# Performance work log

Hardware: AMD Instinct MI355X
Metric: run time of the kernel (lower is better)

The kernel has to match this reference:

```python
import jax, jax.numpy as jnp
import numpy as np

D_MODEL = 1024
NUM_HEADS = 16
DEPTH = D_MODEL // NUM_HEADS


def setup_inputs() -> dict:
    key = jax.random.key(0)
    ks = jax.random.split(key, 8)
    B, S, D = 2, 2048, D_MODEL
    s = 1.0 / np.sqrt(D)
    return {
        "q": jax.random.normal(ks[0], (B, S, D), jnp.float32),
        "k": jax.random.normal(ks[1], (B, S, D), jnp.float32),
        "v": jax.random.normal(ks[2], (B, S, D), jnp.float32),
        "Wq": jax.random.normal(ks[3], (D, D), jnp.float32) * s,
        "bq": jnp.zeros((D,), jnp.float32),
        "Wk": jax.random.normal(ks[4], (D, D), jnp.float32) * s,
        "bk": jnp.zeros((D,), jnp.float32),
        "Wv": jax.random.normal(ks[5], (D, D), jnp.float32) * s,
        "bv": jnp.zeros((D,), jnp.float32),
        "Wo": jax.random.normal(ks[6], (D, D), jnp.float32) * s,
        "bo": jnp.zeros((D,), jnp.float32),
    }


def _split_heads(x):
    # [B,S,D] -> [B,H,S,depth]
    B, S, _ = x.shape
    return x.reshape(B, S, NUM_HEADS, DEPTH).transpose(0, 2, 1, 3)


def reference(q, k, v, Wq, bq, Wk, bk, Wv, bv, Wo, bo):
    qh = _split_heads(q @ Wq + bq)  # [B,H,S,d]
    kh = _split_heads(k @ Wk + bk)
    vh = _split_heads(v @ Wv + bv)
    scale = 1.0 / jnp.sqrt(jnp.float32(DEPTH))
    logits = jnp.einsum("bhqd,bhkd->bhqk", qh, kh) * scale  # [B,H,S,S]
    weights = jax.nn.softmax(logits, axis=-1)
    attn = jnp.einsum("bhqk,bhkd->bhqd", weights, vh)
    B, H, S, d = attn.shape
    attn = attn.transpose(0, 2, 1, 3).reshape(B, S, H * d)  # [B,S,D]
    return attn @ Wo + bo
```

## Files before the change

### kernel.cpp

```cpp
#include <hip/hip_runtime.h>
#include <hip/hip_bf16.h>
#include <stdint.h>


typedef __attribute__((ext_vector_type(8))) short bf16x8;
typedef __attribute__((ext_vector_type(4))) float f32x4;

#define MFMA16(a, b, c) __builtin_amdgcn_mfma_f32_16x16x32_bf16((a), (b), (c), 0, 0, 0)
#define EXP2(x) __builtin_amdgcn_exp2f(x)

static constexpr int S_LEN = 2048;
static constexpr int DM    = 1024;
static constexpr int DEPTH = 64;
static constexpr float QSCALE = 0.125f * 1.44269504088896340736f;

__device__ __forceinline__ unsigned short f2b(float f) {
  unsigned u = __float_as_uint(f);
  unsigned r = 0x7FFFu + ((u >> 16) & 1u);
  return (unsigned short)((u + r) >> 16);
}

__device__ __forceinline__ unsigned short b16(float f) {
  __hip_bfloat16 h = __float2bfloat16(f);
  union { __hip_bfloat16 h; unsigned short u; } c; c.h = h; return c.u;
}

__device__ __forceinline__ void gload16(const void* g, void* l) {
  __builtin_amdgcn_global_load_lds(
      (const __attribute__((address_space(1))) void*)g,
      (__attribute__((address_space(3))) void*)l, 16, 0, 0);
}

__device__ __forceinline__ void wave_lds_fence() {
  asm volatile("" ::: "memory");
  __builtin_amdgcn_sched_barrier(0);
}

__global__ __launch_bounds__(256) void prep_k(
    const float* __restrict__ xq, const float* __restrict__ xk,
    const float* __restrict__ xv, unsigned short* __restrict__ Xb,
    const float* __restrict__ Wq, const float* __restrict__ Wk,
    const float* __restrict__ Wv, const float* __restrict__ Wo,
    unsigned short* __restrict__ Wt) {
  __shared__ unsigned short ts[64][68];
  const int bid = blockIdx.x;
  const int tid = threadIdx.x;
  if (bid < 6144) {
    const int which = bid >> 11;
    const int xb = bid & 2047;
    const float* X = (which == 0) ? xq : (which == 1) ? xk : xv;
    size_t gid = ((size_t)xb * 256 + tid) * 8;
    float4 v0 = *(const float4*)&X[gid];
    float4 v1 = *(const float4*)&X[gid + 4];
    union { unsigned short u[8]; bf16x8 v; } pk;
    pk.u[0] = f2b(v0.x); pk.u[1] = f2b(v0.y); pk.u[2] = f2b(v0.z); pk.u[3] = f2b(v0.w);
    pk.u[4] = f2b(v1.x); pk.u[5] = f2b(v1.y); pk.u[6] = f2b(v1.z); pk.u[7] = f2b(v1.w);
    *(bf16x8*)&Xb[(size_t)which * 4096 * DM + gid] = pk.v;
    return;
  }
  const int wb = bid - 6144;
  const int w = wb >> 8, tile = wb & 255;
  const int tr = tile >> 4, tc = tile & 15;
  const float* W = (w == 0) ? Wq : (w == 1) ? Wk : (w == 2) ? Wv : Wo;
  unsigned short* T = Wt + (size_t)w * DM * DM;
  const int kr = tid >> 4, nc = (tid & 15) * 4;
  #pragma unroll
  for (int j = 0; j < 4; ++j) {
    int k = tr * 64 + kr + j * 16;
    float4 v = *(const float4*)&W[(size_t)k * DM + tc * 64 + nc];
    ushort4 u; u.x = f2b(v.x); u.y = f2b(v.y); u.z = f2b(v.z); u.w = f2b(v.w);
    *(ushort4*)&ts[kr + j * 16][nc] = u;
  }
  __syncthreads();
  const int nr = tid >> 4, kc = (tid & 15) * 4;
  #pragma unroll
  for (int j = 0; j < 4; ++j) {
    int n = tc * 64 + nr + j * 16;
    ushort4 u;
    u.x = ts[kc + 0][nr + j * 16];
    u.y = ts[kc + 1][nr + j * 16];
    u.z = ts[kc + 2][nr + j * 16];
    u.w = ts[kc + 3][nr + j * 16];
    *(ushort4*)&T[(size_t)n * DM + tr * 64 + kc] = u;
  }
}

__global__ __launch_bounds__(256, 4) void proj_qkv_k(
    const unsigned short* __restrict__ Xb, const unsigned short* __restrict__ Wt,
    const float* __restrict__ bq, const float* __restrict__ bk, const float* __restrict__ bv,
    unsigned short* __restrict__ Qh, unsigned short* __restrict__ Kh,
    unsigned short* __restrict__ Vt) {
  __shared__ __align__(16) unsigned short As[2][128][32];
  __shared__ __align__(16) unsigned short Bs[2][128][32];

  const int z = blockIdx.z;
  const unsigned short* A  = Xb + (size_t)z * 4096 * DM;
  const unsigned short* Bt = Wt + (size_t)z * DM * DM;
  const float* bias = (z == 0) ? bq : (z == 1) ? bk : bv;
  const float scale = (z == 0) ? QSCALE : 1.0f;
  unsigned short* O = (z == 0) ? Qh : (z == 1) ? Kh : Vt;

  const int bm = blockIdx.x, bn = blockIdx.y;
  const int tid = threadIdx.x;
  const int wave = tid >> 6, lane = tid & 63;
  const int wr = wave >> 1, wc = wave & 1;
  const int g = lane >> 4, i16 = lane & 15;
  const int srow = tid >> 2, sslot = tid & 3;

  f32x4 acc[4][4] = {};

  auto stage = [&](int ks, int buf) {
    #pragma unroll
    for (int rnd = 0; rnd < 2; ++rnd) {
      int row = rnd * 64 + srow;
      int sw = sslot ^ ((row >> 1) & 3);
      gload16(&A[(size_t)(bm * 128 + row) * DM + ks * 32 + sw * 8],
              &As[buf][row][sslot * 8]);
      gload16(&Bt[(size_t)(bn * 128 + row) * DM + ks * 32 + sw * 8],
              &Bs[buf][row][sslot * 8]);
    }
  };
  auto compute = [&](int buf) {
    bf16x8 a[4], b[4];
    #pragma unroll
    for (int m = 0; m < 4; ++m) {
      int row = wr * 64 + m * 16 + i16;
      int sl = g ^ ((row >> 1) & 3);
      a[m] = *(const bf16x8*)&As[buf][row][sl * 8];
    }
    #pragma unroll
    for (int n = 0; n < 4; ++n) {
      int row = wc * 64 + n * 16 + i16;
      int sl = g ^ ((row >> 1) & 3);
      b[n] = *(const bf16x8*)&Bs[buf][row][sl * 8];
    }
    #pragma unroll
    for (int m = 0; m < 4; ++m)
      #pragma unroll
      for (int n = 0; n < 4; ++n)
        acc[m][n] = MFMA16(a[m], b[n], acc[m][n]);
  };

  stage(0, 0);
  __syncthreads();
  int cur = 0;
  #pragma unroll 1
  for (int ks = 0; ks < DM / 32; ++ks) {
    if (ks + 1 < DM / 32) stage(ks + 1, cur ^ 1);
    compute(cur);
    __syncthreads();
    cur ^= 1;
  }

  #pragma unroll
  for (int m = 0; m < 4; ++m) {
    #pragma unroll
    for (int n = 0; n < 4; ++n) {
      #pragma unroll
      for (int r = 0; r < 4; ++r) {
        int row = bm * 128 + wr * 64 + m * 16 + g * 4 + r;
        int col = bn * 128 + wc * 64 + n * 16 + i16;
        float v = (acc[m][n][r] + bias[col]) * scale;
        int b_ = row >> 11, s = row & 2047;
        int h = col >> 6, dd = col & 63;
        if (z != 2)
          O[(((size_t)(b_ * 16 + h)) * S_LEN + s) * DEPTH + dd] = f2b(v);
        else
          O[(((size_t)(b_ * 16 + h)) * DEPTH + dd) * S_LEN + s] = f2b(v);
      }
    }
  }
}

__global__ __launch_bounds__(256, 4) void out_proj_k(
    const unsigned short* __restrict__ At, const unsigned short* __restrict__ Wto,
    const float* __restrict__ bo, float* __restrict__ out) {
  __shared__ __align__(16) unsigned short As[2][64][32];
  __shared__ __align__(16) unsigned short Bs[2][128][32];

  const int bm = blockIdx.x, bn = blockIdx.y;
  const int tid = threadIdx.x;
  const int wave = tid >> 6, lane = tid & 63;
  const int wr = wave >> 1, wc = wave & 1;
  const int g = lane >> 4, i16 = lane & 15;
  const int srow = tid >> 2, sslot = tid & 3;

  f32x4 acc[2][4] = {};

  auto stage = [&](int ks, int buf) {
    {
      int sw = sslot ^ ((srow >> 1) & 3);
      gload16(&At[(size_t)(bm * 64 + srow) * DM + ks * 32 + sw * 8],
              &As[buf][srow][sslot * 8]);
    }
    #pragma unroll
    for (int rnd = 0; rnd < 2; ++rnd) {
      int row = rnd * 64 + srow;
      int sw = sslot ^ ((row >> 1) & 3);
      gload16(&Wto[(size_t)(bn * 128 + row) * DM + ks * 32 + sw * 8],
              &Bs[buf][row][sslot * 8]);
    }
  };
  auto compute = [&](int buf) {
    bf16x8 a[2], b[4];
    #pragma unroll
    for (int m = 0; m < 2; ++m) {
      int row = wr * 32 + m * 16 + i16;
      int sl = g ^ ((row >> 1) & 3);
      a[m] = *(const bf16x8*)&As[buf][row][sl * 8];
    }
    #pragma unroll
    for (int n = 0; n < 4; ++n) {
      int row = wc * 64 + n * 16 + i16;
      int sl = g ^ ((row >> 1) & 3);
      b[n] = *(const bf16x8*)&Bs[buf][row][sl * 8];
    }
    #pragma unroll
    for (int m = 0; m < 2; ++m)
      #pragma unroll
      for (int n = 0; n < 4; ++n)
        acc[m][n] = MFMA16(a[m], b[n], acc[m][n]);
  };

  stage(0, 0);
  __syncthreads();
  int cur = 0;
  #pragma unroll 1
  for (int ks = 0; ks < DM / 32; ++ks) {
    if (ks + 1 < DM / 32) stage(ks + 1, cur ^ 1);
    compute(cur);
    __syncthreads();
    cur ^= 1;
  }

  #pragma unroll
  for (int m = 0; m < 2; ++m) {
    #pragma unroll
    for (int n = 0; n < 4; ++n) {
      #pragma unroll
      for (int r = 0; r < 4; ++r) {
        int row = bm * 64 + wr * 32 + m * 16 + g * 4 + r;
        int col = bn * 128 + wc * 64 + n * 16 + i16;
        out[(size_t)row * DM + col] = acc[m][n][r] + bo[col];
      }
    }
  }
}

__global__ __launch_bounds__(256) void attn_k(
    const unsigned short* __restrict__ Qh, const unsigned short* __restrict__ Kh,
    const unsigned short* __restrict__ Vt, unsigned short* __restrict__ Ob) {
  __shared__ unsigned short kv_lds[2][2][64][64];
  __shared__ unsigned short p_lds[4][16][64];

  const int linear = blockIdx.y * 32 + blockIdx.x;
  const int wg = (linear & 7) * 128 + (linear >> 3);
  const int qt = wg & 31, bh = wg >> 5;

  const int tid = threadIdx.x;
  const int wave = tid >> 6, lane = tid & 63;
  const int g = lane >> 4, i16 = lane & 15;

  const unsigned short* Q = Qh + (size_t)bh * S_LEN * DEPTH;
  const unsigned short* K = Kh + (size_t)bh * S_LEN * DEPTH;
  const unsigned short* V = Vt + (size_t)bh * DEPTH * S_LEN;

  const int sr0 = tid >> 3;
  const int ss0 = tid & 7;

  const int qbase = qt * 64 + wave * 16;
  const bf16x8 qa0 = *(const bf16x8*)&Q[(size_t)(qbase + i16) * DEPTH + g * 8];
  const bf16x8 qa1 = *(const bf16x8*)&Q[(size_t)(qbase + i16) * DEPTH + 32 + g * 8];

  const short one_b = (short)0x3F80;
  const bf16x8 ones = {one_b, one_b, one_b, one_b, one_b, one_b, one_b, one_b};

  f32x4 l_acc = {0.f, 0.f, 0.f, 0.f};
  f32x4 o[4] = {};

  #pragma unroll
  for (int j = 0; j < 2; ++j) {
    int r = j * 32 + sr0;
    int sw = ss0 ^ (r & 7);
    gload16(&K[(size_t)r * DEPTH + sw * 8], &kv_lds[0][0][r][ss0 * 8]);
    gload16(&V[(size_t)r * S_LEN + sw * 8], &kv_lds[0][1][r][ss0 * 8]);
  }
  __syncthreads();

  int cur = 0;
  #pragma unroll 1
  for (int t64 = 0; t64 < 32; ++t64) {
    const int kv0 = t64 * 64;
    if (t64 + 1 < 32) {
      const int nkv = kv0 + 64;
      #pragma unroll
      for (int j = 0; j < 2; ++j) {
        int r = j * 32 + sr0;
        int sw = ss0 ^ (r & 7);
        gload16(&K[(size_t)(nkv + r) * DEPTH + sw * 8], &kv_lds[cur ^ 1][0][r][ss0 * 8]);
        gload16(&V[(size_t)r * S_LEN + nkv + sw * 8],   &kv_lds[cur ^ 1][1][r][ss0 * 8]);
      }
    }

    f32x4 sT[4];
    const f32x4 zero = {0.f, 0.f, 0.f, 0.f};
    __builtin_amdgcn_s_setprio(1);
    #pragma unroll
    for (int t = 0; t < 4; ++t) {
      int row = t * 16 + i16;
      int x = row & 7;
      bf16x8 k0 = *(const bf16x8*)&kv_lds[cur][0][row][(g ^ x) * 8];
      bf16x8 k1 = *(const bf16x8*)&kv_lds[cur][0][row][((4 + g) ^ x) * 8];
      f32x4 s = MFMA16(k0, qa0, zero);
      sT[t] = MFMA16(k1, qa1, s);
    }
    __builtin_amdgcn_s_setprio(0);

    bf16x8 vf0[4], vf1[4];
    #pragma unroll
    for (int dt = 0; dt < 4; ++dt) {
      int row = dt * 16 + i16;
      int x = row & 7;
      vf0[dt] = *(const bf16x8*)&kv_lds[cur][1][row][(g ^ x) * 8];
      vf1[dt] = *(const bf16x8*)&kv_lds[cur][1][row][((4 + g) ^ x) * 8];
    }

    #pragma unroll
    for (int t = 0; t < 4; ++t) {
      ushort4 w;
      w.x = b16(EXP2(sT[t][0]));
      w.y = b16(EXP2(sT[t][1]));
      w.z = b16(EXP2(sT[t][2]));
      w.w = b16(EXP2(sT[t][3]));
      int idx = (((t * 2 + (g >> 1)) ^ (i16 & 7)) * 8) + (g & 1) * 4;
      *(ushort4*)&p_lds[wave][i16][idx] = w;
    }
    wave_lds_fence();
    bf16x8 pa0 = *(const bf16x8*)&p_lds[wave][i16][(g ^ (i16 & 7)) * 8];
    bf16x8 pa1 = *(const bf16x8*)&p_lds[wave][i16][((4 + g) ^ (i16 & 7)) * 8];

    __builtin_amdgcn_s_setprio(1);
    #pragma unroll
    for (int dt = 0; dt < 4; ++dt) {
      o[dt] = MFMA16(pa0, vf0[dt], o[dt]);
      o[dt] = MFMA16(pa1, vf1[dt], o[dt]);
    }
    l_acc = MFMA16(pa0, ones, l_acc);
    l_acc = MFMA16(pa1, ones, l_acc);
    __builtin_amdgcn_s_setprio(0);

    __syncthreads();
    cur ^= 1;
  }

  const int b_ = bh >> 4, h = bh & 15;
  f32x4 rinv;
  #pragma unroll
  for (int r = 0; r < 4; ++r)
    rinv[r] = 1.0f / l_acc[r];
  #pragma unroll
  for (int dt = 0; dt < 4; ++dt) {
    #pragma unroll
    for (int r = 0; r < 4; ++r) {
      int qrow = qbase + g * 4 + r;
      float val = o[dt][r] * rinv[r];
      Ob[((size_t)(b_ * S_LEN + qrow)) * DM + h * DEPTH + dt * 16 + i16] = f2b(val);
    }
  }
}

extern "C" void kernel_launch(void* const* d_in, const int* in_sizes, int n_in,
                              void* d_out, int out_size, void* d_ws, size_t ws_size,
                              hipStream_t stream) {
  const float* q  = (const float*)d_in[0];
  const float* k  = (const float*)d_in[1];
  const float* v  = (const float*)d_in[2];
  const float* Wq = (const float*)d_in[3];
  const float* bq = (const float*)d_in[4];
  const float* Wk = (const float*)d_in[5];
  const float* bk = (const float*)d_in[6];
  const float* Wv = (const float*)d_in[7];
  const float* bv = (const float*)d_in[8];
  const float* Wo = (const float*)d_in[9];
  const float* bo = (const float*)d_in[10];
  float* out = (float*)d_out;

  const size_t HEAD_ELEMS = (size_t)2 * 16 * S_LEN * DEPTH;
  unsigned short* Qh = (unsigned short*)d_ws;
  unsigned short* Kh = Qh + HEAD_ELEMS;
  unsigned short* Vt = Kh + HEAD_ELEMS;
  unsigned short* Xb = Vt + HEAD_ELEMS;
  unsigned short* At = Xb;
  unsigned short* Wt = Xb + 3 * HEAD_ELEMS;

  dim3 blk(256);
  hipLaunchKernelGGL(prep_k, dim3(7168), blk, 0, stream,
                     q, k, v, Xb, Wq, Wk, Wv, Wo, Wt);
  hipLaunchKernelGGL(proj_qkv_k, dim3(32, 8, 3), blk, 0, stream,
                     Xb, Wt, bq, bk, bv, Qh, Kh, Vt);
  hipLaunchKernelGGL(attn_k, dim3(32, 32), blk, 0, stream, Qh, Kh, Vt, At);
  hipLaunchKernelGGL(out_proj_k, dim3(64, 8), blk, 0, stream,
                     At, Wt + (size_t)3 * DM * DM, bo, out);
}
```

Baseline: 131.7 us.

## Split attention KV range in two and merge partials in a combine kernel

Splits the key/value sequence of the attention kernel into two halves, each handled by its own workgroup, which doubles the grid. Each workgroup writes unnormalised bf16 partial outputs and fp32 row sums. A new combine kernel adds the two partials, divides by the summed row sum, and writes the head-merged activation for the output projection. This is meant to raise parallelism and latency hiding in attention, at the cost of an extra launch, extra global traffic for the partials, and a little precision lost by storing the partials in bf16.

```diff
diff --git a/kernel.cpp b/kernel.cpp
--- a/kernel.cpp
+++ b/kernel.cpp
@@ -23,6 +23,9 @@
 __device__ __forceinline__ unsigned short b16(float f) {
   __hip_bfloat16 h = __float2bfloat16(f);
   union { __hip_bfloat16 h; unsigned short u; } c; c.h = h; return c.u;
+}
+__device__ __forceinline__ float b2f(unsigned short u) {
+  return __uint_as_float(((unsigned)u) << 16);
 }
 
 __device__ __forceinline__ void gload16(const void* g, void* l) {
@@ -249,13 +252,14 @@
 
 __global__ __launch_bounds__(256) void attn_k(
     const unsigned short* __restrict__ Qh, const unsigned short* __restrict__ Kh,
-    const unsigned short* __restrict__ Vt, unsigned short* __restrict__ Ob) {
+    const unsigned short* __restrict__ Vt,
+    unsigned short* __restrict__ op, float* __restrict__ lp) {
   __shared__ unsigned short kv_lds[2][2][64][64];
   __shared__ unsigned short p_lds[4][16][64];
 
-  const int linear = blockIdx.y * 32 + blockIdx.x;
-  const int wg = (linear & 7) * 128 + (linear >> 3);
-  const int qt = wg & 31, bh = wg >> 5;
+  const int linear = blockIdx.z * 1024 + blockIdx.y * 32 + blockIdx.x;
+  const int wg = (linear & 7) * 256 + (linear >> 3);
+  const int qt = wg & 31, bh = (wg >> 5) & 31, sh = wg >> 10;
 
   const int tid = threadIdx.x;
   const int wave = tid >> 6, lane = tid & 63;
@@ -264,6 +268,10 @@
   const unsigned short* Q = Qh + (size_t)bh * S_LEN * DEPTH;
   const unsigned short* K = Kh + (size_t)bh * S_LEN * DEPTH;
   const unsigned short* V = Vt + (size_t)bh * DEPTH * S_LEN;
+  unsigned short* op_h = op + (size_t)sh * 32 * S_LEN * DEPTH;
+  float* lp_h = lp + (size_t)sh * 32 * S_LEN;
+
+  const int kvbase = sh * 1024;
 
   const int sr0 = tid >> 3;
   const int ss0 = tid & 7;
@@ -282,16 +290,16 @@
   for (int j = 0; j < 2; ++j) {
     int r = j * 32 + sr0;
     int sw = ss0 ^ (r & 7);
-    gload16(&K[(size_t)r * DEPTH + sw * 8], &kv_lds[0][0][r][ss0 * 8]);
-    gload16(&V[(size_t)r * S_LEN + sw * 8], &kv_lds[0][1][r][ss0 * 8]);
+    gload16(&K[(size_t)(kvbase + r) * DEPTH + sw * 8], &kv_lds[0][0][r][ss0 * 8]);
+    gload16(&V[(size_t)r * S_LEN + kvbase + sw * 8],   &kv_lds[0][1][r][ss0 * 8]);
   }
   __syncthreads();
 
   int cur = 0;
   #pragma unroll 1
-  for (int t64 = 0; t64 < 32; ++t64) {
-    const int kv0 = t64 * 64;
-    if (t64 + 1 < 32) {
+  for (int t64 = 0; t64 < 16; ++t64) {
+    const int kv0 = kvbase + t64 * 64;
+    if (t64 + 1 < 16) {
       const int nkv = kv0 + 64;
       #pragma unroll
       for (int j = 0; j < 2; ++j) {
@@ -353,20 +361,38 @@
     cur ^= 1;
   }
 
-  const int b_ = bh >> 4, h = bh & 15;
-  f32x4 rinv;
-  #pragma unroll
-  for (int r = 0; r < 4; ++r)
-    rinv[r] = 1.0f / l_acc[r];
   #pragma unroll
   for (int dt = 0; dt < 4; ++dt) {
     #pragma unroll
     for (int r = 0; r < 4; ++r) {
-      int qrow = qbase + g * 4 + r;
-      float val = o[dt][r] * rinv[r];
-      Ob[((size_t)(b_ * S_LEN + qrow)) * DM + h * DEPTH + dt * 16 + i16] = f2b(val);
-    }
-  }
+      int q = qbase + g * 4 + r;
+      op_h[((size_t)bh * S_LEN + q) * DEPTH + dt * 16 + i16] = b16(o[dt][r]);
+    }
+  }
+  if (i16 == 0) {
+    #pragma unroll
+    for (int r = 0; r < 4; ++r)
+      lp_h[(size_t)bh * S_LEN + qbase + g * 4 + r] = l_acc[r];
+  }
+}
+
+__global__ __launch_bounds__(256) void combine_k(
+    const unsigned short* __restrict__ op0, const unsigned short* __restrict__ op1,
+    const float* __restrict__ lp0, const float* __restrict__ lp1,
+    unsigned short* __restrict__ At) {
+  size_t f = (size_t)blockIdx.x * 256 + threadIdx.x;
+  size_t base = f * 8;
+  bf16x8 a = *(const bf16x8*)&op0[base];
+  bf16x8 b = *(const bf16x8*)&op1[base];
+  int row = (int)(base >> 6);
+  float linv = 1.0f / (lp0[row] + lp1[row]);
+  int bh = row >> 11, q = row & 2047;
+  int b_ = bh >> 4, h = bh & 15;
+  union { unsigned short u[8]; bf16x8 v; } o;
+  #pragma unroll
+  for (int j = 0; j < 8; ++j)
+    o.u[j] = b16((b2f((unsigned short)a[j]) + b2f((unsigned short)b[j])) * linv);
+  *(bf16x8*)&At[((size_t)(b_ * S_LEN + q)) * DM + h * DEPTH + (int)(base & 63)] = o.v;
 }
 
 extern "C" void kernel_launch(void* const* d_in, const int* in_sizes, int n_in,
@@ -390,15 +416,21 @@
   unsigned short* Kh = Qh + HEAD_ELEMS;
   unsigned short* Vt = Kh + HEAD_ELEMS;
   unsigned short* Xb = Vt + HEAD_ELEMS;
-  unsigned short* At = Xb;
   unsigned short* Wt = Xb + 3 * HEAD_ELEMS;
+  unsigned short* op0 = Xb;
+  unsigned short* op1 = Xb + HEAD_ELEMS;
+  float* lp = (float*)(Xb + 2 * HEAD_ELEMS);
+  unsigned short* At = Qh;
 
   dim3 blk(256);
   hipLaunchKernelGGL(prep_k, dim3(7168), blk, 0, stream,
                      q, k, v, Xb, Wq, Wk, Wv, Wo, Wt);
   hipLaunchKernelGGL(proj_qkv_k, dim3(32, 8, 3), blk, 0, stream,
                      Xb, Wt, bq, bk, bv, Qh, Kh, Vt);
-  hipLaunchKernelGGL(attn_k, dim3(32, 32), blk, 0, stream, Qh, Kh, Vt, At);
+  hipLaunchKernelGGL(attn_k, dim3(32, 32, 2), blk, 0, stream,
+                     Qh, Kh, Vt, op0, lp);
+  hipLaunchKernelGGL(combine_k, dim3(2048), blk, 0, stream,
+                     op0, op1, lp, lp + 32 * S_LEN, At);
   hipLaunchKernelGGL(out_proj_k, dim3(64, 8), blk, 0, stream,
                      At, Wt + (size_t)3 * DM * DM, bo, out);
 }
```

New measurement: 138.9 us. +5.5%, slower.
